# Optimization experiments

Hardware: AMD Instinct MI355X
Metric: run time of the kernel (lower is better)

## Reference

```python
import jax, jax.numpy as jnp
import numpy as np

B, S, IN_DIM, HID, H, CS = 4, 4096, 1024, 1024, 16, 16
HD = HID // H
LN_EPS = 1e-5


def setup_inputs() -> dict:
    key = jax.random.key(0)
    ks = jax.random.split(key, 6)
    x = jax.random.normal(ks[0], (B, S, IN_DIM), jnp.float32)
    W_in = jax.random.normal(ks[1], (HID, IN_DIM), jnp.float32) * (IN_DIM ** -0.5)
    ln_g = jnp.ones((HID,), jnp.float32)
    ln_b = jnp.zeros((HID,), jnp.float32)
    W_gate = jax.random.normal(ks[2], (2 * H, HID), jnp.float32) * (HID ** -0.5)
    b_gate = jnp.zeros((2 * H,), jnp.float32)
    raw = 0.5 * float(np.log(1.9 / 0.1))  # atanh(0.9), as in _init_eigenvalues
    eig_raw = jnp.full((H,), raw, jnp.float32) + 0.01 * jax.random.normal(ks[3], (H,), jnp.float32)
    W_out = jax.random.normal(ks[4], (HID, HID), jnp.float32) * (HID ** -0.5)
    return {"x": x, "W_in": W_in, "ln_g": ln_g, "ln_b": ln_b,
            "W_gate": W_gate, "b_gate": b_gate, "eig_raw": eig_raw, "W_out": W_out}


def _chunk_scan(a, b):
    # a: (B,S,H) decay, b: (B,S,H,HD) input; h_t = a_t*h_{t-1} + b_t, h0 = 0
    Bsz, Sl = a.shape[0], a.shape[1]
    N = Sl // CS  # seq_len chosen divisible by chunk_size (pad_len == 0)
    ac = a.reshape(Bsz, N, CS, H)
    bc = b.reshape(Bsz, N, CS, H, HD)
    cum = jnp.cumprod(ac, axis=2)  # (B,N,C,H)
    ones = jnp.ones((Bsz, N, 1, H), a.dtype)
    cum_pad = jnp.concatenate([ones, cum[:, :, :-1]], axis=2)  # shifted cumprod
    # M[i,j] = cum_i / cum_pad_j for i>j, 1 on diag, 0 above
    Mi = cum[:, :, :, None, :]        # (B,N,C,1,H)
    Mj = cum_pad[:, :, None, :, :]    # (B,N,1,C,H)
    M = jnp.where(jnp.abs(Mj) > 1e-8, Mi / Mj, jnp.zeros_like(Mi))
    tril = jnp.tril(jnp.ones((CS, CS), a.dtype))[None, None, :, :, None]
    eye = jnp.eye(CS, dtype=a.dtype)[None, None, :, :, None]
    M = M * tril
    M = M * (1 - eye) + eye  # force exact 1 on diagonal
    # within-chunk contribution: (B,N,C,H,HD)
    h_contrib = jnp.einsum('bnijh,bnjhd->bnihd', M, bc)
    # inter-chunk sequential carry
    cum_T = jnp.moveaxis(cum, 1, 0)            # (N,B,C,H)
    hc_T = jnp.moveaxis(h_contrib, 1, 0)       # (N,B,C,H,HD)

    def step(h, inp):
        cum_n, hc_n = inp
        h_chunk = cum_n[..., None] * h[:, None] + hc_n  # (B,C,H,HD)
        return h_chunk[:, -1], h_chunk

    h0 = jnp.zeros((Bsz, H, HD), a.dtype)
    _, h_all = jax.lax.scan(step, h0, (cum_T, hc_T))   # (N,B,C,H,HD)
    h_all = jnp.moveaxis(h_all, 0, 1).reshape(Bsz, Sl, HID)
    return h_all


def reference(x, W_in, ln_g, ln_b, W_gate, b_gate, eig_raw, W_out):
    Bsz, Sl, _ = x.shape
    xp = x @ W_in.T                               # (B,S,HID)
    mu = jnp.mean(xp, axis=-1, keepdims=True)
    var = jnp.mean((xp - mu) ** 2, axis=-1, keepdims=True)
    xp = (xp - mu) * jax.lax.rsqrt(var + LN_EPS) * ln_g + ln_b
    gates = xp @ W_gate.T + b_gate                # (B,S,2H)
    alpha = jax.nn.sigmoid(gates[..., :H])
    beta = jax.nn.sigmoid(gates[..., H:])
    eig = jnp.tanh(eig_raw)                       # (H,)
    a = eig[None, None, :] * alpha                # (B,S,H)
    x_heads = xp.reshape(Bsz, Sl, H, HD)
    b = beta[..., None] * x_heads                 # (B,S,H,HD)
    h_all = _chunk_scan(a, b)                     # (B,S,HID)
    output = h_all @ W_out.T                      # dropout is identity in eval
    h_final = h_all[:, -1, :]
    return output, h_final
```

## Files before the change

kernel.cpp:

```cpp
#include <hip/hip_runtime.h>
#include <hip/hip_bf16.h>
#include <stdint.h>

#define BATCH 4
#define SEQ   4096
#define HID   1024
#define NH    16
#define HD    64
#define CS    16
#define NCH   256
#define MROWS 16384

typedef __attribute__((ext_vector_type(8))) __bf16 bf16x8;
typedef __attribute__((ext_vector_type(4))) float  f32x4;

__device__ __forceinline__ unsigned short f2bf(float f) {
    union { float f; unsigned u; } x; x.f = f;
    unsigned r = x.u + 0x7FFFu + ((x.u >> 16) & 1u);
    return (unsigned short)(r >> 16);
}
__device__ __forceinline__ float bf2f(unsigned short v) {
    union { unsigned u; float f; } x; x.u = ((unsigned)v) << 16;
    return x.f;
}

__device__ __forceinline__ void async_copy16(void* lds, const void* g) {
    __builtin_amdgcn_global_load_lds(
        (const __attribute__((address_space(1))) unsigned int*)g,
        (__attribute__((address_space(3))) unsigned int*)lds,
        16, 0, 0);
}

__global__ __launch_bounds__(256) void convert_all_kernel(
    const float* __restrict__ x, const float* __restrict__ W_in,
    const float* __restrict__ W_out, const float* __restrict__ W_gate,
    unsigned short* __restrict__ xb, unsigned short* __restrict__ Wib,
    unsigned short* __restrict__ Wob, unsigned short* __restrict__ Wgb)
{
    int i = blockIdx.x * 256 + threadIdx.x;
    const float4* src; ushort4* dst; int j;
    if (i < 4194304)      { src = (const float4*)x;      dst = (ushort4*)xb;  j = i; }
    else if (i < 4456448) { src = (const float4*)W_in;   dst = (ushort4*)Wib; j = i - 4194304; }
    else if (i < 4718592) { src = (const float4*)W_out;  dst = (ushort4*)Wob; j = i - 4456448; }
    else if (i < 4726784) { src = (const float4*)W_gate; dst = (ushort4*)Wgb; j = i - 4718592; }
    else return;
    float4 v = src[j];
    ushort4 o;
    o.x = f2bf(v.x); o.y = f2bf(v.y); o.z = f2bf(v.z); o.w = f2bf(v.w);
    dst[j] = o;
}

__global__ __launch_bounds__(256, 2) void gemm_bt_kernel(
    const unsigned short* __restrict__ A,
    const unsigned short* __restrict__ Bm,
    float* __restrict__ C, int M, int N, int K)
{
    __shared__ unsigned short As[128 * 64];
    __shared__ unsigned short Bs[128 * 64];
    const int t = threadIdx.x;
    const int lane = t & 63, w = t >> 6;
    const int wm = w >> 1, wn = w & 1;
    const size_t bm = (size_t)blockIdx.x * 128;
    const size_t bn = (size_t)blockIdx.y * 128;

    f32x4 acc[4][4];
#pragma unroll
    for (int x = 0; x < 4; x++)
#pragma unroll
        for (int y = 0; y < 4; y++)
            acc[x][y] = (f32x4){0.f, 0.f, 0.f, 0.f};

    const int srow = lane >> 3;
    const int gc   = (lane & 7) ^ (srow & 7);
    const int scol = gc * 8;
    const unsigned short* Ag = A + (bm + w * 32 + srow) * (size_t)K + scol;
    const unsigned short* Bg = Bm + (bn + w * 32 + srow) * (size_t)K + scol;
    unsigned short* Al = As + (w * 32 + srow) * 64 + (lane & 7) * 8;
    unsigned short* Bl = Bs + (w * 32 + srow) * 64 + (lane & 7) * 8;

    const int fr = lane & 15, fq = lane >> 4;
    const int rl = fr & 7;

    for (int k0 = 0; k0 < K; k0 += 64) {
#pragma unroll
        for (int r = 0; r < 4; r++) {
            async_copy16(Al + r * 8 * 64, Ag + (size_t)r * 8 * K + k0);
            async_copy16(Bl + r * 8 * 64, Bg + (size_t)r * 8 * K + k0);
        }
        __syncthreads();
#pragma unroll
        for (int kk = 0; kk < 64; kk += 32) {
            const int c = (kk >> 3) + fq;
            const int pc = c ^ rl;
            bf16x8 af[4], bfv[4];
#pragma unroll
            for (int x = 0; x < 4; x++) {
                af[x]  = *(const bf16x8*)(As + (wm * 64 + x * 16 + fr) * 64 + pc * 8);
                bfv[x] = *(const bf16x8*)(Bs + (wn * 64 + x * 16 + fr) * 64 + pc * 8);
            }
#pragma unroll
            for (int x = 0; x < 4; x++)
#pragma unroll
                for (int y = 0; y < 4; y++)
                    acc[x][y] = __builtin_amdgcn_mfma_f32_16x16x32_bf16(af[x], bfv[y], acc[x][y], 0, 0, 0);
        }
        __syncthreads();
    }

#pragma unroll
    for (int x = 0; x < 4; x++) {
#pragma unroll
        for (int y = 0; y < 4; y++) {
            size_t r0 = bm + wm * 64 + x * 16 + fq * 4;
            size_t c  = bn + wn * 64 + y * 16 + fr;
#pragma unroll
            for (int rg = 0; rg < 4; rg++)
                C[(r0 + rg) * (size_t)N + c] = acc[x][y][rg];
        }
    }
}

__global__ __launch_bounds__(256) void mid_kernel(
    const float* __restrict__ xp,
    const float* __restrict__ ln_g, const float* __restrict__ ln_b,
    const unsigned short* __restrict__ Wgb,
    const float* __restrict__ bg, const float* __restrict__ eig_raw,
    unsigned short* __restrict__ xln,
    float* __restrict__ beta_buf,
    float* __restrict__ cum_out,
    float* __restrict__ c15c,
    float* __restrict__ hc15)
{
    __shared__ unsigned short sx[16][1032];
    __shared__ float red[4][2][64][4];
    __shared__ float sg[16][32];
    __shared__ float scum[16][16];
    const int t = threadIdx.x, lane = t & 63, w = t >> 6;
    const int bn = blockIdx.x;
    const size_t m0 = (size_t)(bn >> 8) * SEQ + (size_t)(bn & 255) * 16;

    const int r = t >> 4, u = t & 15;
    {
        const float* row = xp + (m0 + r) * 1024;
        float4 v[16];
        float s = 0.f, s2 = 0.f;
#pragma unroll
        for (int i = 0; i < 16; i++) {
            v[i] = *(const float4*)(row + u * 4 + i * 64);
            s  += v[i].x + v[i].y + v[i].z + v[i].w;
            s2 += v[i].x * v[i].x + v[i].y * v[i].y + v[i].z * v[i].z + v[i].w * v[i].w;
        }
#pragma unroll
        for (int off = 1; off < 16; off <<= 1) {
            s  += __shfl_xor(s, off, 64);
            s2 += __shfl_xor(s2, off, 64);
        }
        const float mu = s * (1.f / 1024.f);
        const float var = s2 * (1.f / 1024.f) - mu * mu;
        const float sc = rsqrtf(var + 1e-5f);
        unsigned short* orow = xln + (m0 + r) * 1024;
#pragma unroll
        for (int i = 0; i < 16; i++) {
            const int k = u * 4 + i * 64;
            float4 g4 = *(const float4*)(ln_g + k);
            float4 b4 = *(const float4*)(ln_b + k);
            ushort4 o;
            o.x = f2bf((v[i].x - mu) * sc * g4.x + b4.x);
            o.y = f2bf((v[i].y - mu) * sc * g4.y + b4.y);
            o.z = f2bf((v[i].z - mu) * sc * g4.z + b4.z);
            o.w = f2bf((v[i].w - mu) * sc * g4.w + b4.w);
            *(ushort4*)&sx[r][k] = o;
            *(ushort4*)(orow + k) = o;
        }
    }
    __syncthreads();

    const int fr = lane & 15, fq = lane >> 4;
    {
        f32x4 acc0 = (f32x4){0.f,0.f,0.f,0.f}, acc1 = (f32x4){0.f,0.f,0.f,0.f};
        const unsigned short* Wr0 = Wgb + (size_t)fr * 1024;
        const unsigned short* Wr1 = Wgb + (size_t)(16 + fr) * 1024;
#pragma unroll
        for (int ks = 0; ks < 8; ks++) {
            const int k0 = w * 256 + ks * 32 + fq * 8;
            bf16x8 af = *(const bf16x8*)&sx[fr][k0];
            bf16x8 b0 = *(const bf16x8*)(Wr0 + k0);
            bf16x8 b1 = *(const bf16x8*)(Wr1 + k0);
            acc0 = __builtin_amdgcn_mfma_f32_16x16x32_bf16(af, b0, acc0, 0, 0, 0);
            acc1 = __builtin_amdgcn_mfma_f32_16x16x32_bf16(af, b1, acc1, 0, 0, 0);
        }
        *(f32x4*)&red[w][0][lane][0] = acc0;
        *(f32x4*)&red[w][1][lane][0] = acc1;
    }
    __syncthreads();
    if (t < 128) {
        const int y = t >> 6, l = t & 63;
        f32x4 s = *(const f32x4*)&red[0][y][l][0];
#pragma unroll
        for (int ww = 1; ww < 4; ww++) {
            f32x4 p = *(const f32x4*)&red[ww][y][l][0];
            s[0] += p[0]; s[1] += p[1]; s[2] += p[2]; s[3] += p[3];
        }
        const int col = y * 16 + (l & 15);
        const int row0 = (l >> 4) * 4;
        const float bias = bg[col];
#pragma unroll
        for (int rg = 0; rg < 4; rg++)
            sg[row0 + rg][col] = 1.f / (1.f + expf(-(s[rg] + bias)));
    }
    __syncthreads();

    if (t < 16) {
        const float ev = tanhf(eig_raw[t]);
        float c = 1.f;
#pragma unroll
        for (int i = 0; i < 16; i++) { c *= ev * sg[i][t]; scum[i][t] = c; }
    }
    beta_buf[(m0 + r) * 16 + u] = sg[r][16 + u];
    __syncthreads();

    cum_out[(size_t)bn * 256 + t] = scum[t >> 4][t & 15];
    if (t < 16) c15c[bn * 16 + t] = scum[15][t];

    {
        const int h = t >> 4, d0 = (t & 15) * 4;
        float s0 = 0.f, s1 = 0.f, s2 = 0.f, s3 = 0.f;
        float b0 = 0.f, b1 = 0.f, b2 = 0.f, b3 = 0.f;
        float cprev = 1.f;
#pragma unroll
        for (int j = 0; j < 16; j++) {
            const float bt = sg[j][16 + h];
            ushort4 xv = *(const ushort4*)&sx[j][h * 64 + d0];
            b0 = bt * bf2f(xv.x); b1 = bt * bf2f(xv.y);
            b2 = bt * bf2f(xv.z); b3 = bt * bf2f(xv.w);
            if (j < 15) {
                const float inv = (fabsf(cprev) > 1e-8f) ? (1.f / cprev) : 0.f;
                s0 += b0 * inv; s1 += b1 * inv; s2 += b2 * inv; s3 += b3 * inv;
                cprev = scum[j][h];
            }
        }
        const float c15 = scum[15][h];
        float4 o = { c15 * s0 + b0, c15 * s1 + b1, c15 * s2 + b2, c15 * s3 + b3 };
        *(float4*)(hc15 + (size_t)bn * 1024 + h * 64 + d0) = o;
    }
}

__global__ __launch_bounds__(256) void scan2a_kernel(
    const float* __restrict__ c15c,
    const float* __restrict__ hc15,
    float* __restrict__ Pg,
    float* __restrict__ Sg)
{
    const int tid = blockIdx.x * 256 + threadIdx.x;
    const int b = tid >> 14, g = (tid >> 10) & 15, hd = tid & 1023, h = hd >> 6;
    const int n0 = b * NCH + g * 16;
    float P = 1.f, S = 0.f;
#pragma unroll
    for (int j = 0; j < 16; j++) {
        const float c = c15c[(n0 + j) * 16 + h];
        S = c * S + hc15[(size_t)(n0 + j) * 1024 + hd];
        P = c * P;
    }
    Pg[tid] = P;
    Sg[tid] = S;
}

__global__ __launch_bounds__(64) void scan2b_kernel(
    const float* __restrict__ Pg, const float* __restrict__ Sg,
    float* __restrict__ GC,
    float* __restrict__ h_final)
{
    const int p = blockIdx.x * 64 + threadIdx.x;
    const int b = p >> 10, hd = p & 1023;
    float gc = 0.f;
#pragma unroll
    for (int g = 0; g < 16; g++) {
        const int idx = (b * 16 + g) * 1024 + hd;
        GC[idx] = gc;
        gc = Pg[idx] * gc + Sg[idx];
    }
    h_final[p] = gc;
}

__global__ __launch_bounds__(256) void scan2c_kernel(
    const float* __restrict__ c15c, const float* __restrict__ hc15,
    const float* __restrict__ GC,
    float* __restrict__ carry_in)
{
    const int tid = blockIdx.x * 256 + threadIdx.x;
    const int b = tid >> 14, g = (tid >> 10) & 15, hd = tid & 1023, h = hd >> 6;
    const int n0 = b * NCH + g * 16;
    float s = GC[tid];
#pragma unroll
    for (int j = 0; j < 16; j++) {
        const size_t bn = n0 + j;
        carry_in[bn * 1024 + hd] = s;
        s = c15c[bn * 16 + h] * s + hc15[bn * 1024 + hd];
    }
}

__global__ __launch_bounds__(256) void scan3_kernel(
    const float* __restrict__ cum_buf,
    const float* __restrict__ beta_buf,
    const unsigned short* __restrict__ xln,
    const float* __restrict__ carry_in,
    unsigned short* __restrict__ hall)
{
    __shared__ float scum[16][16];
    __shared__ float sbeta[16][16];
    const int t = threadIdx.x;
    const int bn = blockIdx.x;
    const size_t m0 = (size_t)(bn >> 8) * SEQ + (size_t)(bn & 255) * 16;

    scum[t >> 4][t & 15]  = cum_buf[(size_t)bn * 256 + t];
    sbeta[t >> 4][t & 15] = beta_buf[(m0 + (t >> 4)) * 16 + (t & 15)];
    __syncthreads();

    const int h = t >> 4, dq = t & 15;
    const size_t off = h * 64 + dq * 4;
    float4 s = *(const float4*)(carry_in + (size_t)bn * 1024 + off);
    float cprev = 1.f;
#pragma unroll
    for (int i = 0; i < 16; i++) {
        ushort4 xv = *(const ushort4*)(xln + (m0 + i) * 1024 + off);
        const float bt = sbeta[i][h];
        const float b0 = bt * bf2f(xv.x), b1 = bt * bf2f(xv.y),
                    b2 = bt * bf2f(xv.z), b3 = bt * bf2f(xv.w);
        const float ci = scum[i][h];
        ushort4 o;
        o.x = f2bf(ci * s.x + b0); o.y = f2bf(ci * s.y + b1);
        o.z = f2bf(ci * s.z + b2); o.w = f2bf(ci * s.w + b3);
        *(ushort4*)(hall + (m0 + i) * 1024 + off) = o;
        const float inv = (fabsf(cprev) > 1e-8f) ? (1.f / cprev) : 0.f;
        s.x += b0 * inv; s.y += b1 * inv; s.z += b2 * inv; s.w += b3 * inv;
        cprev = ci;
    }
}

extern "C" void kernel_launch(void* const* d_in, const int* in_sizes, int n_in,
                              void* d_out, int out_size, void* d_ws, size_t ws_size,
                              hipStream_t stream)
{
    const float* x       = (const float*)d_in[0];
    const float* W_in    = (const float*)d_in[1];
    const float* ln_g    = (const float*)d_in[2];
    const float* ln_b    = (const float*)d_in[3];
    const float* W_gate  = (const float*)d_in[4];
    const float* b_gate  = (const float*)d_in[5];
    const float* eig_raw = (const float*)d_in[6];
    const float* W_out   = (const float*)d_in[7];
    float* out = (float*)d_out;

    char* ws = (char*)d_ws;
    unsigned short* xb   = (unsigned short*)(ws);
    unsigned short* xln  = (unsigned short*)(ws);
    unsigned short* hall = (unsigned short*)(ws + 33554432);
    unsigned short* Wib  = (unsigned short*)(ws + 67108864);
    unsigned short* Wob  = (unsigned short*)(ws + 69206016);
    unsigned short* Wgb  = (unsigned short*)(ws + 71303168);
    float* beta_buf = (float*)(ws + 71368704);
    float* cum_buf  = (float*)(ws + 72417280);
    float* c15c     = (float*)(ws + 73465856);
    float* hc15     = (float*)(ws + 73531392);
    float* carry_in = (float*)(ws + 77725696);

    float* Pg = (float*)(ws + 33554432);
    float* Sg = (float*)(ws + 33554432 + 262144);
    float* GC = (float*)(ws + 33554432 + 524288);

    float* xp = out;
    float* h_final = out + 16777216;

    convert_all_kernel<<<18464, 256, 0, stream>>>(x, W_in, W_out, W_gate, xb, Wib, Wob, Wgb);

    dim3 gg(128, 8);
    gemm_bt_kernel<<<gg, 256, 0, stream>>>(xb, Wib, xp, MROWS, HID, HID);

    mid_kernel<<<1024, 256, 0, stream>>>(xp, ln_g, ln_b, Wgb, b_gate, eig_raw,
                                         xln, beta_buf, cum_buf, c15c, hc15);

    scan2a_kernel<<<256, 256, 0, stream>>>(c15c, hc15, Pg, Sg);
    scan2b_kernel<<<64, 64, 0, stream>>>(Pg, Sg, GC, h_final);
    scan2c_kernel<<<256, 256, 0, stream>>>(c15c, hc15, GC, carry_in);

    scan3_kernel<<<1024, 256, 0, stream>>>(cum_buf, beta_buf, xln, carry_in, hall);

    gemm_bt_kernel<<<gg, 256, 0, stream>>>(hall, Wob, out, MROWS, HID, HID);
}
```

Measured before the change: 255.3 us.

## Widen elementwise kernels to 8-wide accesses and fold scan2b into scan2c

The conversion, layernorm and scan3 kernels now handle 8 elements per thread, using 16-byte bf16 stores and loads in place of 8-byte ones, and scan3 runs with half the threads. The separate scan2b launch is removed: each scan2c thread rebuilds its group carry by serially combining the preceding group prefixes, and the last group writes h_final. This cuts one launch and uses wider memory transactions, at the cost of redundant prefix work in scan2c and fewer threads in flight per block.

```diff
diff --git a/kernel.cpp b/kernel.cpp
--- a/kernel.cpp
+++ b/kernel.cpp
@@ -13,6 +13,7 @@
 
 typedef __attribute__((ext_vector_type(8))) __bf16 bf16x8;
 typedef __attribute__((ext_vector_type(4))) float  f32x4;
+typedef __attribute__((ext_vector_type(8))) unsigned short u16x8;
 
 __device__ __forceinline__ unsigned short f2bf(float f) {
     union { float f; unsigned u; } x; x.f = f;
@@ -38,15 +39,16 @@
     unsigned short* __restrict__ Wob, unsigned short* __restrict__ Wgb)
 {
     int i = blockIdx.x * 256 + threadIdx.x;
-    const float4* src; ushort4* dst; int j;
-    if (i < 4194304)      { src = (const float4*)x;      dst = (ushort4*)xb;  j = i; }
-    else if (i < 4456448) { src = (const float4*)W_in;   dst = (ushort4*)Wib; j = i - 4194304; }
-    else if (i < 4718592) { src = (const float4*)W_out;  dst = (ushort4*)Wob; j = i - 4456448; }
-    else if (i < 4726784) { src = (const float4*)W_gate; dst = (ushort4*)Wgb; j = i - 4718592; }
+    const float4* src; u16x8* dst; int j;
+    if (i < 2097152)      { src = (const float4*)x;      dst = (u16x8*)xb;  j = i; }
+    else if (i < 2228224) { src = (const float4*)W_in;   dst = (u16x8*)Wib; j = i - 2097152; }
+    else if (i < 2359296) { src = (const float4*)W_out;  dst = (u16x8*)Wob; j = i - 2228224; }
+    else if (i < 2363392) { src = (const float4*)W_gate; dst = (u16x8*)Wgb; j = i - 2359296; }
     else return;
-    float4 v = src[j];
-    ushort4 o;
-    o.x = f2bf(v.x); o.y = f2bf(v.y); o.z = f2bf(v.z); o.w = f2bf(v.w);
+    float4 a = src[2 * j], b = src[2 * j + 1];
+    u16x8 o;
+    o[0] = f2bf(a.x); o[1] = f2bf(a.y); o[2] = f2bf(a.z); o[3] = f2bf(a.w);
+    o[4] = f2bf(b.x); o[5] = f2bf(b.y); o[6] = f2bf(b.z); o[7] = f2bf(b.w);
     dst[j] = o;
 }
 
@@ -142,13 +144,17 @@
     const int r = t >> 4, u = t & 15;
     {
         const float* row = xp + (m0 + r) * 1024;
-        float4 v[16];
+        float4 va[8], vb[8];
         float s = 0.f, s2 = 0.f;
 #pragma unroll
-        for (int i = 0; i < 16; i++) {
-            v[i] = *(const float4*)(row + u * 4 + i * 64);
-            s  += v[i].x + v[i].y + v[i].z + v[i].w;
-            s2 += v[i].x * v[i].x + v[i].y * v[i].y + v[i].z * v[i].z + v[i].w * v[i].w;
+        for (int i = 0; i < 8; i++) {
+            const int k = u * 8 + i * 128;
+            va[i] = *(const float4*)(row + k);
+            vb[i] = *(const float4*)(row + k + 4);
+            s  += va[i].x + va[i].y + va[i].z + va[i].w
+                + vb[i].x + vb[i].y + vb[i].z + vb[i].w;
+            s2 += va[i].x * va[i].x + va[i].y * va[i].y + va[i].z * va[i].z + va[i].w * va[i].w
+                + vb[i].x * vb[i].x + vb[i].y * vb[i].y + vb[i].z * vb[i].z + vb[i].w * vb[i].w;
         }
 #pragma unroll
         for (int off = 1; off < 16; off <<= 1) {
@@ -160,17 +166,23 @@
         const float sc = rsqrtf(var + 1e-5f);
         unsigned short* orow = xln + (m0 + r) * 1024;
 #pragma unroll
-        for (int i = 0; i < 16; i++) {
-            const int k = u * 4 + i * 64;
-            float4 g4 = *(const float4*)(ln_g + k);
-            float4 b4 = *(const float4*)(ln_b + k);
-            ushort4 o;
-            o.x = f2bf((v[i].x - mu) * sc * g4.x + b4.x);
-            o.y = f2bf((v[i].y - mu) * sc * g4.y + b4.y);
-            o.z = f2bf((v[i].z - mu) * sc * g4.z + b4.z);
-            o.w = f2bf((v[i].w - mu) * sc * g4.w + b4.w);
-            *(ushort4*)&sx[r][k] = o;
-            *(ushort4*)(orow + k) = o;
+        for (int i = 0; i < 8; i++) {
+            const int k = u * 8 + i * 128;
+            float4 g4a = *(const float4*)(ln_g + k);
+            float4 g4b = *(const float4*)(ln_g + k + 4);
+            float4 b4a = *(const float4*)(ln_b + k);
+            float4 b4b = *(const float4*)(ln_b + k + 4);
+            u16x8 o;
+            o[0] = f2bf((va[i].x - mu) * sc * g4a.x + b4a.x);
+            o[1] = f2bf((va[i].y - mu) * sc * g4a.y + b4a.y);
+            o[2] = f2bf((va[i].z - mu) * sc * g4a.z + b4a.z);
+            o[3] = f2bf((va[i].w - mu) * sc * g4a.w + b4a.w);
+            o[4] = f2bf((vb[i].x - mu) * sc * g4b.x + b4b.x);
+            o[5] = f2bf((vb[i].y - mu) * sc * g4b.y + b4b.y);
+            o[6] = f2bf((vb[i].z - mu) * sc * g4b.z + b4b.z);
+            o[7] = f2bf((vb[i].w - mu) * sc * g4b.w + b4b.w);
+            *(u16x8*)&sx[r][k] = o;
+            *(u16x8*)(orow + k) = o;
         }
     }
     __syncthreads();
@@ -265,41 +277,30 @@
     Sg[tid] = S;
 }
 
-__global__ __launch_bounds__(64) void scan2b_kernel(
-    const float* __restrict__ Pg, const float* __restrict__ Sg,
-    float* __restrict__ GC,
-    float* __restrict__ h_final)
-{
-    const int p = blockIdx.x * 64 + threadIdx.x;
-    const int b = p >> 10, hd = p & 1023;
-    float gc = 0.f;
-#pragma unroll
-    for (int g = 0; g < 16; g++) {
-        const int idx = (b * 16 + g) * 1024 + hd;
-        GC[idx] = gc;
-        gc = Pg[idx] * gc + Sg[idx];
-    }
-    h_final[p] = gc;
-}
-
 __global__ __launch_bounds__(256) void scan2c_kernel(
     const float* __restrict__ c15c, const float* __restrict__ hc15,
-    const float* __restrict__ GC,
-    float* __restrict__ carry_in)
+    const float* __restrict__ Pg, const float* __restrict__ Sg,
+    float* __restrict__ carry_in,
+    float* __restrict__ h_final)
 {
     const int tid = blockIdx.x * 256 + threadIdx.x;
     const int b = tid >> 14, g = (tid >> 10) & 15, hd = tid & 1023, h = hd >> 6;
     const int n0 = b * NCH + g * 16;
-    float s = GC[tid];
+    float s = 0.f;
+    for (int gp = 0; gp < g; gp++) {
+        const int idx = ((b * 16 + gp) << 10) + hd;
+        s = Pg[idx] * s + Sg[idx];
+    }
 #pragma unroll
     for (int j = 0; j < 16; j++) {
         const size_t bn = n0 + j;
         carry_in[bn * 1024 + hd] = s;
         s = c15c[bn * 16 + h] * s + hc15[bn * 1024 + hd];
     }
-}
-
-__global__ __launch_bounds__(256) void scan3_kernel(
+    if (g == 15) h_final[(b << 10) + hd] = s;
+}
+
+__global__ __launch_bounds__(128) void scan3_kernel(
     const float* __restrict__ cum_buf,
     const float* __restrict__ beta_buf,
     const unsigned short* __restrict__ xln,
@@ -312,27 +313,38 @@
     const int bn = blockIdx.x;
     const size_t m0 = (size_t)(bn >> 8) * SEQ + (size_t)(bn & 255) * 16;
 
-    scum[t >> 4][t & 15]  = cum_buf[(size_t)bn * 256 + t];
-    sbeta[t >> 4][t & 15] = beta_buf[(m0 + (t >> 4)) * 16 + (t & 15)];
-    __syncthreads();
-
-    const int h = t >> 4, dq = t & 15;
-    const size_t off = h * 64 + dq * 4;
-    float4 s = *(const float4*)(carry_in + (size_t)bn * 1024 + off);
+    {
+        const int i0 = t, i1 = t + 128;
+        scum[i0 >> 4][i0 & 15]  = cum_buf[(size_t)bn * 256 + i0];
+        scum[i1 >> 4][i1 & 15]  = cum_buf[(size_t)bn * 256 + i1];
+        sbeta[i0 >> 4][i0 & 15] = beta_buf[(m0 + (i0 >> 4)) * 16 + (i0 & 15)];
+        sbeta[i1 >> 4][i1 & 15] = beta_buf[(m0 + (i1 >> 4)) * 16 + (i1 & 15)];
+    }
+    __syncthreads();
+
+    const int h = t >> 3, dq = t & 7;
+    const size_t off = h * 64 + dq * 8;
+    float s[8];
+    *(float4*)&s[0] = *(const float4*)(carry_in + (size_t)bn * 1024 + off);
+    *(float4*)&s[4] = *(const float4*)(carry_in + (size_t)bn * 1024 + off + 4);
     float cprev = 1.f;
 #pragma unroll
     for (int i = 0; i < 16; i++) {
-        ushort4 xv = *(const ushort4*)(xln + (m0 + i) * 1024 + off);
+        u16x8 xv = *(const u16x8*)(xln + (m0 + i) * 1024 + off);
         const float bt = sbeta[i][h];
-        const float b0 = bt * bf2f(xv.x), b1 = bt * bf2f(xv.y),
-                    b2 = bt * bf2f(xv.z), b3 = bt * bf2f(xv.w);
         const float ci = scum[i][h];
-        ushort4 o;
-        o.x = f2bf(ci * s.x + b0); o.y = f2bf(ci * s.y + b1);
-        o.z = f2bf(ci * s.z + b2); o.w = f2bf(ci * s.w + b3);
-        *(ushort4*)(hall + (m0 + i) * 1024 + off) = o;
+        float bb[8];
+        u16x8 o;
+#pragma unroll
+        for (int e = 0; e < 8; e++) {
+            bb[e] = bt * bf2f(xv[e]);
+            o[e] = f2bf(ci * s[e] + bb[e]);
+        }
+        *(u16x8*)(hall + (m0 + i) * 1024 + off) = o;
         const float inv = (fabsf(cprev) > 1e-8f) ? (1.f / cprev) : 0.f;
-        s.x += b0 * inv; s.y += b1 * inv; s.z += b2 * inv; s.w += b3 * inv;
+#pragma unroll
+        for (int e = 0; e < 8; e++)
+            s[e] += bb[e] * inv;
         cprev = ci;
     }
 }
@@ -366,12 +378,11 @@
 
     float* Pg = (float*)(ws + 33554432);
     float* Sg = (float*)(ws + 33554432 + 262144);
-    float* GC = (float*)(ws + 33554432 + 524288);
 
     float* xp = out;
     float* h_final = out + 16777216;
 
-    convert_all_kernel<<<18464, 256, 0, stream>>>(x, W_in, W_out, W_gate, xb, Wib, Wob, Wgb);
+    convert_all_kernel<<<9232, 256, 0, stream>>>(x, W_in, W_out, W_gate, xb, Wib, Wob, Wgb);
 
     dim3 gg(128, 8);
     gemm_bt_kernel<<<gg, 256, 0, stream>>>(xb, Wib, xp, MROWS, HID, HID);
@@ -380,10 +391,9 @@
                                          xln, beta_buf, cum_buf, c15c, hc15);
 
     scan2a_kernel<<<256, 256, 0, stream>>>(c15c, hc15, Pg, Sg);
-    scan2b_kernel<<<64, 64, 0, stream>>>(Pg, Sg, GC, h_final);
-    scan2c_kernel<<<256, 256, 0, stream>>>(c15c, hc15, GC, carry_in);
-
-    scan3_kernel<<<1024, 256, 0, stream>>>(cum_buf, beta_buf, xln, carry_in, hall);
+    scan2c_kernel<<<256, 256, 0, stream>>>(c15c, hc15, Pg, Sg, carry_in, h_final);
+
+    scan3_kernel<<<1024, 128, 0, stream>>>(cum_buf, beta_buf, xln, carry_in, hall);
 
     gemm_bt_kernel<<<gg, 256, 0, stream>>>(hall, Wob, out, MROWS, HID, HID);
 }
```

Measured after the change: 253.5 us. No clear change (-0.7%).
